# Performance work log

Measured on AMD Instinct MI355X. Metric: run time of the kernel, lower is better.

Reference implementation:

```python
import jax, jax.numpy as jnp
import numpy as np

N = 100000
E = 300000
IN_C = 256
HID = 256   # 2 * out_channels
OUT_C = 128


def setup_inputs() -> dict:
    key = jax.random.key(0)
    k1, k2, k3, k4, k5 = jax.random.split(key, 5)
    x = jax.random.normal(k1, (N, IN_C), dtype=jnp.float32)
    edge_index = jax.random.randint(k2, (2, E), 0, N, dtype=jnp.int64)
    # Glorot-style init scale for GEMM weights
    W1 = jax.random.normal(k3, (IN_C, HID), dtype=jnp.float32) * (1.0 / np.sqrt(IN_C))
    b1 = jnp.zeros((HID,), dtype=jnp.float32)
    W2 = jax.random.normal(k4, (HID, OUT_C), dtype=jnp.float32) * (1.0 / np.sqrt(HID))
    b2 = jnp.zeros((OUT_C,), dtype=jnp.float32)
    return {"x": x, "edge_index": edge_index, "W1": W1, "b1": b1, "W2": W2, "b2": b2}


def _gcn_conv(x, W, b, src, dst, norm, n_nodes):
    # x: [N, Fin] -> transform then gather-scale-scatter aggregate
    h = x @ W                                   # [N, Fout]
    msgs = h[src] * norm[:, None]               # [E+N, Fout] (includes self-loops)
    out = jax.ops.segment_sum(msgs, dst, num_segments=n_nodes)
    return out + b


def _gcn_norm(edge_index, n_nodes):
    # add self-loops, compute symmetric deg^-1/2 normalization (PyG GCNConv default)
    loops = jnp.arange(n_nodes, dtype=edge_index.dtype)
    src = jnp.concatenate([edge_index[0], loops])
    dst = jnp.concatenate([edge_index[1], loops])
    deg = jax.ops.segment_sum(jnp.ones_like(dst, dtype=jnp.float32), dst, num_segments=n_nodes)
    dinv = jnp.where(deg > 0, jax.lax.rsqrt(deg), 0.0)
    norm = dinv[src] * dinv[dst]                # [E+N]
    return src, dst, norm


def reference(x, edge_index, W1, b1, W2, b2):
    n_nodes = x.shape[0]
    src, dst, norm = _gcn_norm(edge_index, n_nodes)
    h = _gcn_conv(x, W1, b1, src, dst, norm, n_nodes)
    h = jax.nn.relu(h)
    # dropout is identity in eval mode (reference baseline runs deterministic eval)
    return _gcn_conv(h, W2, b2, src, dst, norm, n_nodes)
```

## Files before the change

### kernel.cpp

```cpp
#include <hip/hip_runtime.h>
#include <stdint.h>

#define IN_C  256
#define HID   256
#define OUT_C 128
#define SCAN_BS 1024

typedef __bf16 bf16x8 __attribute__((ext_vector_type(8)));
typedef float  f32x4  __attribute__((ext_vector_type(4)));
typedef unsigned short u16x8 __attribute__((ext_vector_type(8)));
typedef unsigned short u16x4 __attribute__((ext_vector_type(4)));
typedef unsigned short u16x2 __attribute__((ext_vector_type(2)));
typedef unsigned int u32;

static __device__ __forceinline__ unsigned short f2b(float f) {
    union { float f; uint32_t u; } v; v.f = f;
    uint32_t r = v.u + 0x7fffu + ((v.u >> 16) & 1u);
    return (unsigned short)(r >> 16);
}
static __device__ __forceinline__ float b2f(unsigned short b) {
    union { uint32_t u; float f; } v; v.u = ((uint32_t)b) << 16;
    return v.f;
}
static __device__ __forceinline__ u32 cvtpk(float lo, float hi) {
    u32 r;
    asm("v_cvt_pk_bf16_f32 %0, %1, %2" : "=v"(r) : "v"(lo), "v"(hi));
    return r;
}

typedef __attribute__((address_space(1))) const u32 gas_u32;
typedef __attribute__((address_space(3))) u32 las_u32;
static __device__ __forceinline__ void gld16(const void* g, void* l) {
    __builtin_amdgcn_global_load_lds((gas_u32*)g, (las_u32*)l, 16, 0, 0);
}

__global__ void k_init(const float* __restrict__ W1, const float* __restrict__ W2,
                       unsigned short* __restrict__ W1G, unsigned short* __restrict__ W2T,
                       int* __restrict__ cnt, int n) {
    int i = blockIdx.x * blockDim.x + threadIdx.x;
    if (i < 65536) {
        int gi = i >> 3, j = i & 7;
        int kt = gi >> 10, c = (gi >> 8) & 3, nn = gi & 255;
        W1G[i] = f2b(W1[(size_t)(kt * 32 + c * 8 + j) * HID + nn]);
    }
    if (i < 32768) W2T[i] = f2b(W2[(i & 255) * OUT_C + (i >> 8)]);
    if (i < n) cnt[i] = 0;
}

__global__ void k_count(const int* __restrict__ dst, int* __restrict__ cnt, int e) {
    int i = blockIdx.x * blockDim.x + threadIdx.x;
    if (i < e) atomicAdd(&cnt[dst[i]], 1);
}

__global__ __launch_bounds__(SCAN_BS) void k_scan_block(
    const int* __restrict__ cnt, int* __restrict__ rs, int* __restrict__ bsum, int n) {
    __shared__ int s[SCAN_BS];
    const int tid = threadIdx.x;
    const int i = blockIdx.x * SCAN_BS + tid;
    int v = (i < n) ? cnt[i] + 1 : 0;
    s[tid] = v;
    __syncthreads();
    for (int off = 1; off < SCAN_BS; off <<= 1) {
        int t = (tid >= off) ? s[tid - off] : 0;
        __syncthreads();
        s[tid] += t;
        __syncthreads();
    }
    if (i < n) rs[i] = s[tid] - v;
    if (tid == SCAN_BS - 1) bsum[blockIdx.x] = s[tid];
}

__global__ void k_scan_sums(int* __restrict__ bsum, int nb) {
    __shared__ int s[128];
    const int tid = threadIdx.x;
    int v = (tid < nb) ? bsum[tid] : 0;
    s[tid] = v;
    __syncthreads();
    for (int off = 1; off < 128; off <<= 1) {
        int t = (tid >= off) ? s[tid - off] : 0;
        __syncthreads();
        s[tid] += t;
        __syncthreads();
    }
    if (tid < nb) bsum[tid] = s[tid] - v;
}

__global__ void k_scan_add(int* __restrict__ rs, int* __restrict__ cur,
                           const int* __restrict__ bsum, const int* __restrict__ cnt,
                           float* __restrict__ dinv, int2* __restrict__ csrw, int n) {
    int i = blockIdx.x * blockDim.x + threadIdx.x;
    if (i < n) {
        int v = rs[i] + bsum[i >> 10];
        rs[i] = v;
        cur[i] = v + 1;
        float dp1 = (float)(cnt[i] + 1);
        dinv[i] = rsqrtf(dp1);
        csrw[v] = make_int2(i, __float_as_int(1.0f / dp1));
    }
}

__global__ void k_fill(const int* __restrict__ src, const int* __restrict__ dst,
                       const float* __restrict__ dinv,
                       int* __restrict__ cur, int2* __restrict__ csrw, int e) {
    int i = blockIdx.x * blockDim.x + threadIdx.x;
    if (i < e) {
        int s = src[i], d = dst[i];
        int p = atomicAdd(&cur[d], 1);
        csrw[p] = make_int2(s, __float_as_int(dinv[s] * dinv[d]));
    }
}

__global__ __launch_bounds__(512) void k_gemm1(
    const float* __restrict__ x, const unsigned short* __restrict__ W1G,
    unsigned short* __restrict__ t1, int n) {
    __shared__ __align__(16) unsigned short As[2][4096];
    __shared__ __align__(16) unsigned short Bs[2][8192];
    const int tid  = threadIdx.x;
    const int row0 = blockIdx.x * 128;
    const int wid = tid >> 6, lane = tid & 63;
    const int wm = wid >> 2, wn = wid & 3;
    const int lrow = lane & 15, lgrp = lane >> 4;

    const int ar = tid & 127, ac = tid >> 7;
    int arow = row0 + ar; if (arow > n - 1) arow = n - 1;
    const float* aptr = x + (size_t)arow * IN_C + ac * 8;

    f32x4 acc[4][4];
    #pragma unroll
    for (int i = 0; i < 4; ++i)
        #pragma unroll
        for (int j = 0; j < 4; ++j)
            acc[i][j] = (f32x4){0.f, 0.f, 0.f, 0.f};

    {
        #pragma unroll
        for (int i = 0; i < 2; ++i) {
            int chunk = tid + 512 * i;
            gld16(&W1G[(size_t)chunk * 8], &Bs[0][chunk * 8]);
        }
        f32x4 a = *(const f32x4*)aptr;
        f32x4 b = *(const f32x4*)(aptr + 4);
        union { u32 w[4]; u16x8 v; } pk;
        pk.w[0] = cvtpk(a[0], a[1]); pk.w[1] = cvtpk(a[2], a[3]);
        pk.w[2] = cvtpk(b[0], b[1]); pk.w[3] = cvtpk(b[2], b[3]);
        *(u16x8*)&As[0][ac * 1024 + ar * 8] = pk.v;
    }
    __syncthreads();

    int cur = 0;
    for (int kt = 0; kt < 8; ++kt) {
        const int nxt = cur ^ 1;
        f32x4 pa, pb;
        const bool more = (kt < 7);
        if (more) {
            #pragma unroll
            for (int i = 0; i < 2; ++i) {
                int chunk = tid + 512 * i;
                gld16(&W1G[(size_t)(kt + 1) * 8192 + chunk * 8], &Bs[nxt][chunk * 8]);
            }
            const float* ap = aptr + (kt + 1) * 32;
            pa = *(const f32x4*)ap;
            pb = *(const f32x4*)(ap + 4);
        }
        bf16x8 av[4], bv[4];
        #pragma unroll
        for (int mf = 0; mf < 4; ++mf) {
            int r = wm * 64 + mf * 16 + lrow;
            av[mf] = *(const bf16x8*)&As[cur][lgrp * 1024 + r * 8];
        }
        #pragma unroll
        for (int nf = 0; nf < 4; ++nf) {
            int cc = wn * 64 + nf * 16 + lrow;
            bv[nf] = *(const bf16x8*)&Bs[cur][lgrp * 2048 + cc * 8];
        }
        #pragma unroll
        for (int mf = 0; mf < 4; ++mf)
            #pragma unroll
            for (int nf = 0; nf < 4; ++nf)
                acc[mf][nf] = __builtin_amdgcn_mfma_f32_16x16x32_bf16(
                    av[mf], bv[nf], acc[mf][nf], 0, 0, 0);
        if (more) {
            union { u32 w[4]; u16x8 v; } pk;
            pk.w[0] = cvtpk(pa[0], pa[1]); pk.w[1] = cvtpk(pa[2], pa[3]);
            pk.w[2] = cvtpk(pb[0], pb[1]); pk.w[3] = cvtpk(pb[2], pb[3]);
            *(u16x8*)&As[nxt][ac * 1024 + ar * 8] = pk.v;
        }
        __syncthreads();
        cur = nxt;
    }

    unsigned short* Cs = &Bs[0][0];
    #pragma unroll
    for (int mf = 0; mf < 4; ++mf) {
        #pragma unroll
        for (int nf = 0; nf < 4; ++nf)
            #pragma unroll
            for (int j = 0; j < 4; ++j)
                Cs[(wm * 16 + lgrp * 4 + j) * 260 + wn * 64 + nf * 16 + lrow] =
                    f2b(acc[mf][nf][j]);
        __syncthreads();
        #pragma unroll
        for (int it = 0; it < 2; ++it) {
            int chunk = tid + 512 * it;
            int lr = chunk >> 5, c8 = chunk & 31;
            u16x8 v = *(const u16x8*)&Cs[lr * 260 + c8 * 8];
            int grow = row0 + (lr >> 4) * 64 + mf * 16 + (lr & 15);
            if (grow < n)
                *(u16x8*)&t1[(size_t)grow * HID + c8 * 8] = v;
        }
        if (mf < 3) __syncthreads();
    }
}

__global__ __launch_bounds__(256) void k_agg1(
    const unsigned short* __restrict__ t1, const int* __restrict__ rs,
    const int* __restrict__ cnt, const int2* __restrict__ csrw,
    const float* __restrict__ b1, unsigned short* __restrict__ out1, int n) {
    const int w = blockIdx.x * 4 + (threadIdx.x >> 6);
    const int n0 = w * 4;
    if (n0 >= n) return;
    const int lane = threadIdx.x & 63;
    const int ch = lane * 4;
    int beg[4], m[4];
    #pragma unroll
    for (int q = 0; q < 4; ++q) {
        int node = n0 + q;
        bool valid = node < n;
        beg[q] = valid ? rs[node] : 0;
        m[q]   = valid ? cnt[node] + 1 : 0;
    }
    float acc[4][4];
    #pragma unroll
    for (int q = 0; q < 4; ++q)
        #pragma unroll
        for (int k = 0; k < 4; ++k) acc[q][k] = 0.f;
    const int m01 = m[0] > m[1] ? m[0] : m[1];
    const int m23 = m[2] > m[3] ? m[2] : m[3];
    const int mmax = m01 > m23 ? m01 : m23;
    for (int j = 0; j < mmax; ++j) {
        #pragma unroll
        for (int q = 0; q < 4; ++q) {
            if (j < m[q]) {
                int2 p = csrw[beg[q] + j];
                float wq = __int_as_float(p.y);
                u16x4 u = *(const u16x4*)&t1[(size_t)p.x * HID + ch];
                acc[q][0] += b2f(u[0]) * wq; acc[q][1] += b2f(u[1]) * wq;
                acc[q][2] += b2f(u[2]) * wq; acc[q][3] += b2f(u[3]) * wq;
            }
        }
    }
    float4 bb = *(const float4*)(b1 + ch);
    #pragma unroll
    for (int q = 0; q < 4; ++q) {
        int node = n0 + q;
        if (node < n) {
            u16x4 o;
            o[0] = f2b(fmaxf(acc[q][0] + bb.x, 0.f));
            o[1] = f2b(fmaxf(acc[q][1] + bb.y, 0.f));
            o[2] = f2b(fmaxf(acc[q][2] + bb.z, 0.f));
            o[3] = f2b(fmaxf(acc[q][3] + bb.w, 0.f));
            *(u16x4*)&out1[(size_t)node * HID + ch] = o;
        }
    }
}

__global__ __launch_bounds__(256) void k_gemm2(
    const unsigned short* __restrict__ out1, const unsigned short* __restrict__ W2T,
    unsigned short* __restrict__ t2, int n) {
    __shared__ __align__(16) unsigned short As[128 * 64];
    __shared__ __align__(16) unsigned short Bs[128 * 64];
    const int tid  = threadIdx.x;
    const int row0 = blockIdx.x * 128;
    const int wid = tid >> 6, lane = tid & 63;
    const int wm = wid >> 1, wn = wid & 1;
    const int lrow = lane & 15, lgrp = lane >> 4;

    f32x4 acc[4][4];
    #pragma unroll
    for (int i = 0; i < 4; ++i)
        #pragma unroll
        for (int j = 0; j < 4; ++j)
            acc[i][j] = (f32x4){0.f, 0.f, 0.f, 0.f};

    for (int kt = 0; kt < 4; ++kt) {
        #pragma unroll
        for (int i = 0; i < 4; ++i) {
            int chunk = tid + 256 * i;
            int r = chunk >> 3, c = chunk & 7;
            int grow = row0 + r; if (grow > n - 1) grow = n - 1;
            gld16(&out1[(size_t)grow * HID + kt * 64 + ((c ^ (r & 7)) * 8)],
                  &As[chunk * 8]);
        }
        #pragma unroll
        for (int i = 0; i < 4; ++i) {
            int chunk = tid + 256 * i;
            int nn = chunk >> 3, c = chunk & 7;
            gld16(&W2T[(size_t)nn * 256 + kt * 64 + ((c ^ (nn & 7)) * 8)],
                  &Bs[chunk * 8]);
        }
        __syncthreads();
        #pragma unroll
        for (int kk = 0; kk < 2; ++kk) {
            const int cfrag = kk * 4 + lgrp;
            bf16x8 av[4], bv[4];
            #pragma unroll
            for (int mf = 0; mf < 4; ++mf) {
                int r = wm * 64 + mf * 16 + lrow;
                av[mf] = *(const bf16x8*)&As[r * 64 + ((cfrag ^ (r & 7)) * 8)];
            }
            #pragma unroll
            for (int nf = 0; nf < 4; ++nf) {
                int cc = wn * 64 + nf * 16 + lrow;
                bv[nf] = *(const bf16x8*)&Bs[cc * 64 + ((cfrag ^ (cc & 7)) * 8)];
            }
            #pragma unroll
            for (int mf = 0; mf < 4; ++mf)
                #pragma unroll
                for (int nf = 0; nf < 4; ++nf)
                    acc[mf][nf] = __builtin_amdgcn_mfma_f32_16x16x32_bf16(
                        av[mf], bv[nf], acc[mf][nf], 0, 0, 0);
        }
        __syncthreads();
    }

    unsigned short* Cs = &Bs[0];
    #pragma unroll
    for (int mf = 0; mf < 4; ++mf) {
        #pragma unroll
        for (int nf = 0; nf < 4; ++nf)
            #pragma unroll
            for (int j = 0; j < 4; ++j)
                Cs[(wm * 16 + lgrp * 4 + j) * 132 + wn * 64 + nf * 16 + lrow] =
                    f2b(acc[mf][nf][j]);
        __syncthreads();
        #pragma unroll
        for (int it = 0; it < 2; ++it) {
            int chunk = tid + 256 * it;
            int lr = chunk >> 4, c8 = chunk & 15;
            u16x8 v = *(const u16x8*)&Cs[lr * 132 + c8 * 8];
            int grow = row0 + (lr >> 4) * 64 + mf * 16 + (lr & 15);
            if (grow < n)
                *(u16x8*)&t2[(size_t)grow * OUT_C + c8 * 8] = v;
        }
        if (mf < 3) __syncthreads();
    }
}

__global__ __launch_bounds__(256) void k_agg2(
    const unsigned short* __restrict__ t2, const int* __restrict__ rs,
    const int* __restrict__ cnt, const int2* __restrict__ csrw,
    const float* __restrict__ b2, float* __restrict__ out, int n) {
    const int w = blockIdx.x * 4 + (threadIdx.x >> 6);
    const int n0 = w * 4;
    if (n0 >= n) return;
    const int lane = threadIdx.x & 63;
    const int ch = lane * 2;
    int beg[4], m[4];
    #pragma unroll
    for (int q = 0; q < 4; ++q) {
        int node = n0 + q;
        bool valid = node < n;
        beg[q] = valid ? rs[node] : 0;
        m[q]   = valid ? cnt[node] + 1 : 0;
    }
    float acc[4][2];
    #pragma unroll
    for (int q = 0; q < 4; ++q) { acc[q][0] = 0.f; acc[q][1] = 0.f; }
    const int m01 = m[0] > m[1] ? m[0] : m[1];
    const int m23 = m[2] > m[3] ? m[2] : m[3];
    const int mmax = m01 > m23 ? m01 : m23;
    for (int j = 0; j < mmax; ++j) {
        #pragma unroll
        for (int q = 0; q < 4; ++q) {
            if (j < m[q]) {
                int2 p = csrw[beg[q] + j];
                float wq = __int_as_float(p.y);
                u16x2 u = *(const u16x2*)&t2[(size_t)p.x * OUT_C + ch];
                acc[q][0] += b2f(u[0]) * wq; acc[q][1] += b2f(u[1]) * wq;
            }
        }
    }
    float2 bb = *(const float2*)(b2 + ch);
    #pragma unroll
    for (int q = 0; q < 4; ++q) {
        int node = n0 + q;
        if (node < n)
            *(float2*)&out[(size_t)node * OUT_C + ch] =
                make_float2(acc[q][0] + bb.x, acc[q][1] + bb.y);
    }
}

extern "C" void kernel_launch(void* const* d_in, const int* in_sizes, int n_in,
                              void* d_out, int out_size, void* d_ws, size_t ws_size,
                              hipStream_t stream) {
    const float* x  = (const float*)d_in[0];
    const int*   ei = (const int*)d_in[1];
    const float* W1 = (const float*)d_in[2];
    const float* b1 = (const float*)d_in[3];
    const float* W2 = (const float*)d_in[4];
    const float* b2 = (const float*)d_in[5];
    float* out = (float*)d_out;

    const int n = in_sizes[0] / IN_C;
    const int e = in_sizes[1] / 2;
    const int* src = ei;
    const int* dst = ei + e;

    int*   cnt  = (int*)d_ws;
    int*   rs   = cnt + n;
    int*   cur  = rs + n;
    int*   bsum = cur + n;
    float* dinv = (float*)(bsum + 128);
    int2*  csrw = (int2*)(dinv + n);
    unsigned short* W1G = (unsigned short*)(csrw + (size_t)e + n);
    unsigned short* W2T = W1G + 65536;
    unsigned short* t1  = W2T + 32768;
    unsigned short* out1 = t1 + (size_t)n * HID;
    unsigned short* t2  = t1;

    const int nb = (n + SCAN_BS - 1) / SCAN_BS;

    k_init<<<(n + 255) / 256, 256, 0, stream>>>(W1, W2, W1G, W2T, cnt, n);
    k_count<<<(e + 255) / 256, 256, 0, stream>>>(dst, cnt, e);
    k_scan_block<<<nb, SCAN_BS, 0, stream>>>(cnt, rs, bsum, n);
    k_scan_sums<<<1, 128, 0, stream>>>(bsum, nb);
    k_scan_add<<<(n + 255) / 256, 256, 0, stream>>>(rs, cur, bsum, cnt, dinv, csrw, n);
    k_fill<<<(e + 255) / 256, 256, 0, stream>>>(src, dst, dinv, cur, csrw, e);

    const int mb = (n + 127) / 128;
    k_gemm1<<<mb, 512, 0, stream>>>(x, W1G, t1, n);
    const int aggblk = (n + 15) / 16;
    k_agg1<<<aggblk, 256, 0, stream>>>(t1, rs, cnt, csrw, b1, out1, n);
    k_gemm2<<<mb, 256, 0, stream>>>(out1, W2T, t2, n);
    k_agg2<<<aggblk, 256, 0, stream>>>(t2, rs, cnt, csrw, b2, out, n);
}
```

Baseline: 208.3 us.

## Triple-buffer W1 tiles in gemm1 with explicit vmcnt waits and sched barriers

Moves the B-operand (W1) staging in the first GEMM from double to triple buffering, prefetching two K-tiles ahead via global_load_lds. The loop is fully unrolled, and __syncthreads is replaced by hand-placed s_waitcnt vmcnt(2) plus s_barrier, so only the oldest loads are waited on. Sched barriers pin the instruction order. This aims to hide global load latency behind MFMA work, at the cost of 16 KB more LDS, which may reduce occupancy.

```diff
diff --git a/kernel.cpp b/kernel.cpp
--- a/kernel.cpp
+++ b/kernel.cpp
@@ -33,6 +33,7 @@
 static __device__ __forceinline__ void gld16(const void* g, void* l) {
     __builtin_amdgcn_global_load_lds((gas_u32*)g, (las_u32*)l, 16, 0, 0);
 }
+#define SB() __builtin_amdgcn_sched_barrier(0)
 
 __global__ void k_init(const float* __restrict__ W1, const float* __restrict__ W2,
                        unsigned short* __restrict__ W1G, unsigned short* __restrict__ W2T,
@@ -114,7 +115,7 @@
     const float* __restrict__ x, const unsigned short* __restrict__ W1G,
     unsigned short* __restrict__ t1, int n) {
     __shared__ __align__(16) unsigned short As[2][4096];
-    __shared__ __align__(16) unsigned short Bs[2][8192];
+    __shared__ __align__(16) unsigned short Bs[3][8192];
     const int tid  = threadIdx.x;
     const int row0 = blockIdx.x * 128;
     const int wid = tid >> 6, lane = tid & 63;
@@ -133,45 +134,60 @@
             acc[i][j] = (f32x4){0.f, 0.f, 0.f, 0.f};
 
     {
+        f32x4 a = *(const f32x4*)aptr;
+        f32x4 b = *(const f32x4*)(aptr + 4);
+        SB();
         #pragma unroll
         for (int i = 0; i < 2; ++i) {
             int chunk = tid + 512 * i;
             gld16(&W1G[(size_t)chunk * 8], &Bs[0][chunk * 8]);
         }
-        f32x4 a = *(const f32x4*)aptr;
-        f32x4 b = *(const f32x4*)(aptr + 4);
+        #pragma unroll
+        for (int i = 0; i < 2; ++i) {
+            int chunk = tid + 512 * i;
+            gld16(&W1G[(size_t)8192 + chunk * 8], &Bs[1][chunk * 8]);
+        }
+        SB();
         union { u32 w[4]; u16x8 v; } pk;
         pk.w[0] = cvtpk(a[0], a[1]); pk.w[1] = cvtpk(a[2], a[3]);
         pk.w[2] = cvtpk(b[0], b[1]); pk.w[3] = cvtpk(b[2], b[3]);
         *(u16x8*)&As[0][ac * 1024 + ar * 8] = pk.v;
-    }
-    __syncthreads();
-
-    int cur = 0;
-    for (int kt = 0; kt < 8; ++kt) {
-        const int nxt = cur ^ 1;
+        asm volatile("s_waitcnt vmcnt(2) lgkmcnt(0)" ::: "memory");
+        SB();
+        __builtin_amdgcn_s_barrier();
+        SB();
+    }
+
+    #pragma unroll
+    for (int t = 0; t < 8; ++t) {
+        const int cb = t % 3;
+        const int ca = t & 1;
         f32x4 pa, pb;
-        const bool more = (kt < 7);
-        if (more) {
+        if (t < 7) {
+            const float* ap = aptr + (t + 1) * 32;
+            pa = *(const f32x4*)ap;
+            pb = *(const f32x4*)(ap + 4);
+        }
+        SB();
+        if (t < 6) {
+            const int nb3 = (t + 2) % 3;
             #pragma unroll
             for (int i = 0; i < 2; ++i) {
                 int chunk = tid + 512 * i;
-                gld16(&W1G[(size_t)(kt + 1) * 8192 + chunk * 8], &Bs[nxt][chunk * 8]);
+                gld16(&W1G[(size_t)(t + 2) * 8192 + chunk * 8], &Bs[nb3][chunk * 8]);
             }
-            const float* ap = aptr + (kt + 1) * 32;
-            pa = *(const f32x4*)ap;
-            pb = *(const f32x4*)(ap + 4);
-        }
+        }
+        SB();
         bf16x8 av[4], bv[4];
         #pragma unroll
         for (int mf = 0; mf < 4; ++mf) {
             int r = wm * 64 + mf * 16 + lrow;
-            av[mf] = *(const bf16x8*)&As[cur][lgrp * 1024 + r * 8];
+            av[mf] = *(const bf16x8*)&As[ca][lgrp * 1024 + r * 8];
         }
         #pragma unroll
         for (int nf = 0; nf < 4; ++nf) {
             int cc = wn * 64 + nf * 16 + lrow;
-            bv[nf] = *(const bf16x8*)&Bs[cur][lgrp * 2048 + cc * 8];
+            bv[nf] = *(const bf16x8*)&Bs[cb][lgrp * 2048 + cc * 8];
         }
         #pragma unroll
         for (int mf = 0; mf < 4; ++mf)
@@ -179,16 +195,23 @@
             for (int nf = 0; nf < 4; ++nf)
                 acc[mf][nf] = __builtin_amdgcn_mfma_f32_16x16x32_bf16(
                     av[mf], bv[nf], acc[mf][nf], 0, 0, 0);
-        if (more) {
+        SB();
+        if (t < 7) {
             union { u32 w[4]; u16x8 v; } pk;
             pk.w[0] = cvtpk(pa[0], pa[1]); pk.w[1] = cvtpk(pa[2], pa[3]);
             pk.w[2] = cvtpk(pb[0], pb[1]); pk.w[3] = cvtpk(pb[2], pb[3]);
-            *(u16x8*)&As[nxt][ac * 1024 + ar * 8] = pk.v;
-        }
-        __syncthreads();
-        cur = nxt;
-    }
-
+            *(u16x8*)&As[(t + 1) & 1][ac * 1024 + ar * 8] = pk.v;
+            if (t < 6)
+                asm volatile("s_waitcnt vmcnt(2) lgkmcnt(0)" ::: "memory");
+            else
+                asm volatile("s_waitcnt vmcnt(0) lgkmcnt(0)" ::: "memory");
+            SB();
+            __builtin_amdgcn_s_barrier();
+            SB();
+        }
+    }
+
+    __syncthreads();
     unsigned short* Cs = &Bs[0][0];
     #pragma unroll
     for (int mf = 0; mf < 4; ++mf) {
```

New measurement: 209.8 us. Within noise of the previous version (+0.7%).
